# Optimization experiments

Hardware: AMD Instinct MI355X
Metric: run time of the kernel (lower is better)

## Reference

```python
import jax, jax.numpy as jnp
import numpy as np

N_NODES = 10000   # graph size (pos/field tables, dense adjacency)
FEATS = 32        # node_feats
HEADS = 4         # n_heads
SAMPLES = 256     # n_samples (random mids per endpoint)
SENTINELS = 8     # n_sentinels
N_BATCH = 2048    # edges per forward batch
N_EDGES_G = 100000  # graph edges used to build dense adjacency buffer


def setup_inputs() -> dict:
    key = jax.random.key(0)
    ks = jax.random.split(key, 7)
    edge = jax.random.randint(ks[0], (N_BATCH, 2), 0, N_NODES)
    mid0 = jax.random.randint(ks[1], (HEADS, N_BATCH, SAMPLES), 0, N_NODES)
    mid1 = jax.random.randint(ks[2], (HEADS, N_BATCH, SAMPLES), 0, N_NODES)
    # learned parameters (torch: nn.Parameter(torch.rand(...)), ones*5)
    pos = jax.random.uniform(ks[3], (HEADS, N_NODES, FEATS), dtype=jnp.float32)
    field = jax.random.uniform(ks[4], (HEADS, N_NODES, FEATS), dtype=jnp.float32)
    uncertainty = jnp.ones((1, 1, 1), jnp.float32) * 5.0
    # dense adjacency buffer: -1 everywhere, +1 on (symmetrized) graph edges
    src_g = jax.random.randint(ks[5], (N_EDGES_G,), 0, N_NODES)
    dst_g = jax.random.randint(ks[6], (N_EDGES_G,), 0, N_NODES)
    edge_mat = -jnp.ones((N_NODES, N_NODES), jnp.float32)
    edge_mat = edge_mat.at[src_g, dst_g].set(1.0).at[dst_g, src_g].set(1.0)
    return {"edge": edge, "mid0": mid0, "mid1": mid1, "pos": pos,
            "field": field, "uncertainty": uncertainty, "edge_mat": edge_mat}


def reference(edge, mid0, mid1, pos, field, uncertainty, edge_mat):
    src, dst = edge[:, 0], edge[:, 1]
    h = jnp.arange(HEADS)[:, None, None]           # head index for gathers
    # gather sampled mid-node positions and form difference vectors
    srcdiff = pos[:, src][:, :, None, :] - pos[h, mid0]   # (H, n, S, F)
    dstdiff = pos[:, dst][:, :, None, :] - pos[h, mid1]   # (H, n, S, F)
    # per-sample dot-product logits + memory bias (memory == -1 branch)
    logits1 = (jnp.einsum('hnsf,hnf->hns', srcdiff, field[:, dst])
               + uncertainty * edge_mat[mid0, dst[None, :, None]])
    logits2 = (jnp.einsum('hnsf,hnf->hns', dstdiff, field[:, src])
               + uncertainty * edge_mat[src[None, :, None], mid1])
    logits = jnp.concatenate([logits1, logits2], axis=2)  # (H, n, 2S)
    dist = jnp.concatenate([jnp.linalg.norm(srcdiff, axis=3),
                            jnp.linalg.norm(dstdiff, axis=3)], axis=2)
    # sentinels: zero logits at unit distance
    n = edge.shape[0]
    logits = jnp.concatenate([logits, jnp.zeros((HEADS, n, SENTINELS), logits.dtype)], axis=2)
    dist = jnp.concatenate([dist, jnp.ones((HEADS, n, SENTINELS), dist.dtype)], axis=2)
    # softmin aggregation: softmax over (1 - dist), weighted sum of logits, mean over heads
    w = jax.nn.softmax(1.0 - dist, axis=2)                # (H, n, 2S+sent)
    return jnp.sum(logits * w, axis=2).mean(0)            # (n,)
```

## Files before the change

kernel.cpp:

```cpp
#include <hip/hip_runtime.h>

#define N_NODES 10000
#define FEATS 32
#define HEADS 4
#define SAMPLES 256
#define N_BATCH 2048
#define NGROUP 40
#define NWORDS (NGROUP * 4)

typedef float f32x4 __attribute__((ext_vector_type(4)));
typedef unsigned long long u64;

#define WS_NEEDED (N_NODES * NWORDS * 8)

__global__ __launch_bounds__(256) void mask_dedup_kernel(
    const int* __restrict__ edge,
    const float* __restrict__ edge_mat,
    u64* __restrict__ mask_table,
    float* __restrict__ out)
{
    const int bid  = blockIdx.x;
    const int tid  = threadIdx.x;
    const int w    = tid >> 6;
    const int lane = tid & 63;

    if (tid == 0 && bid < N_BATCH) out[bid] = 0.f;

    const int v = edge[bid];

    __shared__ int s_dup;
    if (tid == 0) s_dup = 0;
    __syncthreads();
    for (int j = tid; j < bid; j += 256)
        if (edge[j] == v) s_dup = 1;
    __syncthreads();
    if (s_dup) return;

    const float* rp = edge_mat + (size_t)v * N_NODES;
    u64* wsn = mask_table + (size_t)v * NWORDS;

    f32x4 val[10];
    #pragma unroll
    for (int i = 0; i < 10; ++i) {
        const int base = (i * 4 + w) * 256 + lane * 4;
        f32x4 t = {-1.f, -1.f, -1.f, -1.f};
        if (base < N_NODES) t = *(const f32x4*)(rp + base);
        val[i] = t;
    }
    #pragma unroll
    for (int i = 0; i < 10; ++i) {
        const int g = i * 4 + w;
        u64 b0 = __ballot(val[i].x > 0.f);
        u64 b1 = __ballot(val[i].y > 0.f);
        u64 b2 = __ballot(val[i].z > 0.f);
        u64 b3 = __ballot(val[i].w > 0.f);
        if (lane < 4) {
            u64 bb = lane == 0 ? b0 : lane == 1 ? b1 : lane == 2 ? b2 : b3;
            wsn[g * 4 + lane] = bb;
        }
    }
}

__global__ __launch_bounds__(256, 4) void madgraph_kernel(
    const int* __restrict__ edge,
    const int* __restrict__ mid0,
    const int* __restrict__ mid1,
    const float* __restrict__ pos,
    const float* __restrict__ field,
    const float* __restrict__ unc,
    const u64* __restrict__ mask_table,
    float* __restrict__ out)
{
    const int b    = blockIdx.x;
    const int h    = b & 3;
    const int tid  = threadIdx.x;
    const int w    = tid >> 6;
    const int lane = tid & 63;
    const int n    = (b >> 2) + 512 * w;

    __shared__ u64 s_mask[4][2 * NWORDS];

    const int src = edge[2 * n];
    const int dst = edge[2 * n + 1];
    const float U = unc[0];

    const u64* wdst = mask_table + (size_t)dst * NWORDS;
    const u64* wsrc = mask_table + (size_t)src * NWORDS;
    #pragma unroll
    for (int k = 0; k < 5; ++k) {
        const int idx = k * 64 + lane;
        s_mask[w][idx] = (idx < NWORDS) ? wdst[idx] : wsrc[idx - NWORDS];
    }

    const float* posh   = pos   + (size_t)h * N_NODES * FEATS;
    const float* fieldh = field + (size_t)h * N_NODES * FEATS;
    const int q = lane & 3;
    const int g = lane >> 2;

    float4 A[2][2], F[2][2];
    #pragma unroll
    for (int sd = 0; sd < 2; ++sd) {
        const float4* pa = (const float4*)(posh   + (size_t)(sd ? dst : src) * FEATS);
        const float4* pf = (const float4*)(fieldh + (size_t)(sd ? src : dst) * FEATS);
        A[sd][0] = pa[q]; A[sd][1] = pa[q + 4];
        F[sd][0] = pf[q]; F[sd][1] = pf[q + 4];
    }

    const size_t sb = ((size_t)h * N_BATCH + n) * SAMPLES;
    int mm[8];
    #pragma unroll
    for (int c = 0; c < 8; ++c)
        mm[c] = (c < 4 ? mid0 : mid1)[sb + (c & 3) * 64 + lane];

    float num = 0.f, den = 0.f;
    #pragma unroll
    for (int c = 0; c < 8; ++c) {
        const int side = c >> 2;

        int    mArr[4];
        float4 B0[4], B1[4];
        #pragma unroll
        for (int t = 0; t < 4; ++t)
            mArr[t] = __shfl(mm[c], t * 16 + g);
        #pragma unroll
        for (int t = 0; t < 4; ++t) {
            const float4* rp = (const float4*)(posh + (size_t)mArr[t] * FEATS);
            B0[t] = rp[q];
            B1[t] = rp[q + 4];
        }

        #pragma unroll
        for (int t = 0; t < 4; ++t) {
            float dh = 0.f, nh = 0.f;
            {
                float4 a = A[side][0], f = F[side][0];
                float dx = a.x - B0[t].x, dy = a.y - B0[t].y,
                      dz = a.z - B0[t].z, dw = a.w - B0[t].w;
                dh += dx * f.x + dy * f.y + dz * f.z + dw * f.w;
                nh += dx * dx + dy * dy + dz * dz + dw * dw;
            }
            {
                float4 a = A[side][1], f = F[side][1];
                float dx = a.x - B1[t].x, dy = a.y - B1[t].y,
                      dz = a.z - B1[t].z, dw = a.w - B1[t].w;
                dh += dx * f.x + dy * f.y + dz * f.z + dw * f.w;
                nh += dx * dx + dy * dy + dz * dz + dw * dw;
            }
            dh += __shfl_xor(dh, 1); nh += __shfl_xor(nh, 1);
            dh += __shfl_xor(dh, 2); nh += __shfl_xor(nh, 2);

            const u64 wbits =
                s_mask[w][side * NWORDS + ((mArr[t] >> 8) << 2) + (mArr[t] & 3)];
            const float em = ((wbits >> ((mArr[t] >> 2) & 63)) & 1ull) ? U : -U;

            const float wgt = __expf(1.0f - sqrtf(nh));
            num += (dh + em) * wgt;
            den += wgt;
        }
    }

    #pragma unroll
    for (int off = 32; off > 0; off >>= 1) {
        num += __shfl_xor(num, off);
        den += __shfl_xor(den, off);
    }
    if (lane == 0) {
        atomicAdd(out + n, 0.25f * (num / (den + 32.0f)));
    }
}

__global__ __launch_bounds__(256) void mask_kernel(
    const int* __restrict__ edge,
    const float* __restrict__ edge_mat,
    u64* __restrict__ ws_mask,
    float* __restrict__ out)
{
    const int n    = blockIdx.x;
    const int tid  = threadIdx.x;
    const int wave = tid >> 6;
    const int lane = tid & 63;
    const int src = edge[2 * n];
    const int dst = edge[2 * n + 1];
    if (tid == 0) out[n] = 0.f;
    u64* wsn = ws_mask + (size_t)n * 2 * NWORDS;
    #pragma unroll
    for (int r = 0; r < 2; ++r) {
        const float* rp = edge_mat + (size_t)(r ? src : dst) * N_NODES;
        for (int g = wave; g < NGROUP; g += 4) {
            int base = g * 256 + lane * 4;
            float4 v = make_float4(-1.f, -1.f, -1.f, -1.f);
            if (base < N_NODES) v = *(const float4*)(rp + base);
            u64 b0 = __ballot(v.x > 0.f);
            u64 b1 = __ballot(v.y > 0.f);
            u64 b2 = __ballot(v.z > 0.f);
            u64 b3 = __ballot(v.w > 0.f);
            if (lane < 4) {
                u64 bb = lane == 0 ? b0 : lane == 1 ? b1 : lane == 2 ? b2 : b3;
                wsn[r * NWORDS + g * 4 + lane] = bb;
            }
        }
    }
}

__global__ __launch_bounds__(256, 4) void madgraph_kernel_fb(
    const int* __restrict__ edge,
    const int* __restrict__ mid0,
    const int* __restrict__ mid1,
    const float* __restrict__ pos,
    const float* __restrict__ field,
    const float* __restrict__ unc,
    const u64* __restrict__ ws_mask,
    float* __restrict__ out)
{
    const int b    = blockIdx.x;
    const int h    = b & 3;
    const int tid  = threadIdx.x;
    const int w    = tid >> 6;
    const int lane = tid & 63;
    const int n    = (b >> 2) + 512 * w;

    __shared__ u64 s_mask[4][2 * NWORDS];

    const int src = edge[2 * n];
    const int dst = edge[2 * n + 1];
    const float U = unc[0];

    const u64* wsn = ws_mask + (size_t)n * 2 * NWORDS;
    #pragma unroll
    for (int k = 0; k < 5; ++k)
        s_mask[w][k * 64 + lane] = wsn[k * 64 + lane];

    const float* posh   = pos   + (size_t)h * N_NODES * FEATS;
    const float* fieldh = field + (size_t)h * N_NODES * FEATS;
    const int q = lane & 3;
    const int g = lane >> 2;

    float4 A[2][2], F[2][2];
    #pragma unroll
    for (int sd = 0; sd < 2; ++sd) {
        const float4* pa = (const float4*)(posh   + (size_t)(sd ? dst : src) * FEATS);
        const float4* pf = (const float4*)(fieldh + (size_t)(sd ? src : dst) * FEATS);
        A[sd][0] = pa[q]; A[sd][1] = pa[q + 4];
        F[sd][0] = pf[q]; F[sd][1] = pf[q + 4];
    }

    const size_t sb = ((size_t)h * N_BATCH + n) * SAMPLES;
    int mm[8];
    #pragma unroll
    for (int c = 0; c < 8; ++c)
        mm[c] = (c < 4 ? mid0 : mid1)[sb + (c & 3) * 64 + lane];

    float num = 0.f, den = 0.f;
    #pragma unroll
    for (int c = 0; c < 8; ++c) {
        const int side = c >> 2;
        int    mArr[4];
        float4 B0[4], B1[4];
        #pragma unroll
        for (int t = 0; t < 4; ++t)
            mArr[t] = __shfl(mm[c], t * 16 + g);
        #pragma unroll
        for (int t = 0; t < 4; ++t) {
            const float4* rp = (const float4*)(posh + (size_t)mArr[t] * FEATS);
            B0[t] = rp[q];
            B1[t] = rp[q + 4];
        }
        #pragma unroll
        for (int t = 0; t < 4; ++t) {
            float dh = 0.f, nh = 0.f;
            {
                float4 a = A[side][0], f = F[side][0];
                float dx = a.x - B0[t].x, dy = a.y - B0[t].y,
                      dz = a.z - B0[t].z, dw = a.w - B0[t].w;
                dh += dx * f.x + dy * f.y + dz * f.z + dw * f.w;
                nh += dx * dx + dy * dy + dz * dz + dw * dw;
            }
            {
                float4 a = A[side][1], f = F[side][1];
                float dx = a.x - B1[t].x, dy = a.y - B1[t].y,
                      dz = a.z - B1[t].z, dw = a.w - B1[t].w;
                dh += dx * f.x + dy * f.y + dz * f.z + dw * f.w;
                nh += dx * dx + dy * dy + dz * dz + dw * dw;
            }
            dh += __shfl_xor(dh, 1); nh += __shfl_xor(nh, 1);
            dh += __shfl_xor(dh, 2); nh += __shfl_xor(nh, 2);
            const u64 wbits =
                s_mask[w][side * NWORDS + ((mArr[t] >> 8) << 2) + (mArr[t] & 3)];
            const float em = ((wbits >> ((mArr[t] >> 2) & 63)) & 1ull) ? U : -U;
            const float wgt = __expf(1.0f - sqrtf(nh));
            num += (dh + em) * wgt;
            den += wgt;
        }
    }
    #pragma unroll
    for (int off = 32; off > 0; off >>= 1) {
        num += __shfl_xor(num, off);
        den += __shfl_xor(den, off);
    }
    if (lane == 0)
        atomicAdd(out + n, 0.25f * (num / (den + 32.0f)));
}

extern "C" void kernel_launch(void* const* d_in, const int* in_sizes, int n_in,
                              void* d_out, int out_size, void* d_ws, size_t ws_size,
                              hipStream_t stream) {
    const int*   edge     = (const int*)  d_in[0];
    const int*   mid0     = (const int*)  d_in[1];
    const int*   mid1     = (const int*)  d_in[2];
    const float* pos      = (const float*)d_in[3];
    const float* field    = (const float*)d_in[4];
    const float* unc      = (const float*)d_in[5];
    const float* edge_mat = (const float*)d_in[6];
    float*       out      = (float*)d_out;

    if (ws_size >= (size_t)WS_NEEDED) {
        u64* mask_table = (u64*)d_ws;
        mask_dedup_kernel<<<2 * N_BATCH, 256, 0, stream>>>(edge, edge_mat,
                                                           mask_table, out);
        madgraph_kernel<<<N_BATCH, 256, 0, stream>>>(edge, mid0, mid1, pos,
                                                     field, unc, mask_table, out);
    } else {
        u64* ws_mask = (u64*)d_ws;
        mask_kernel<<<N_BATCH, 256, 0, stream>>>(edge, edge_mat, ws_mask, out);
        madgraph_kernel_fb<<<N_BATCH, 256, 0, stream>>>(edge, mid0, mid1, pos,
                                                        field, unc, ws_mask, out);
    }
}
```

Baseline: 58.64 us.

## Gather mid-node positions from an fp16 copy of pos built in the mask kernel

Adds extra blocks to the mask kernel that convert pos to fp16 in workspace each call. The main kernel then gathers mid-node rows as 16-byte fp16 vectors (8 features per lane, 8 samples per batch), halving the random-gather traffic. It also drops the fallback mask kernel path. The cost is an extra full pos conversion pass every call, and the fp16 rounding of pos adds precision error to distances and logits.

Result: slower. 61.13 us (+4.2%).

```diff
diff --git a/kernel.cpp b/kernel.cpp
--- a/kernel.cpp
+++ b/kernel.cpp
@@ -9,20 +9,43 @@
 #define NWORDS (NGROUP * 4)
 
 typedef float f32x4 __attribute__((ext_vector_type(4)));
+typedef _Float16 f16x8 __attribute__((ext_vector_type(8)));
 typedef unsigned long long u64;
 
-#define WS_NEEDED (N_NODES * NWORDS * 8)
+#define WS_P16_OFF  12800000
+#define WS_NEED_V2  15360000
+#define WS_NEED_V1  12800000
+#define POS_ELEMS   (HEADS * N_NODES * FEATS)
 
 __global__ __launch_bounds__(256) void mask_dedup_kernel(
     const int* __restrict__ edge,
     const float* __restrict__ edge_mat,
+    const float* __restrict__ pos,
     u64* __restrict__ mask_table,
-    float* __restrict__ out)
+    _Float16* __restrict__ ws_pos16,
+    float* __restrict__ out,
+    int do_conv)
 {
     const int bid  = blockIdx.x;
     const int tid  = threadIdx.x;
     const int w    = tid >> 6;
     const int lane = tid & 63;
+
+    if (bid >= 2 * N_BATCH) {
+        if (!do_conv) return;
+        const int idx = (bid - 2 * N_BATCH) * 2048 + tid * 8;
+        if (idx < POS_ELEMS) {
+            const float4 v0 = *(const float4*)(pos + idx);
+            const float4 v1 = *(const float4*)(pos + idx + 4);
+            f16x8 o;
+            o[0] = (_Float16)v0.x; o[1] = (_Float16)v0.y;
+            o[2] = (_Float16)v0.z; o[3] = (_Float16)v0.w;
+            o[4] = (_Float16)v1.x; o[5] = (_Float16)v1.y;
+            o[6] = (_Float16)v1.z; o[7] = (_Float16)v1.w;
+            *(f16x8*)(ws_pos16 + idx) = o;
+        }
+        return;
+    }
 
     if (tid == 0 && bid < N_BATCH) out[bid] = 0.f;
 
@@ -61,7 +84,118 @@
     }
 }
 
-__global__ __launch_bounds__(256, 4) void madgraph_kernel(
+__global__ __launch_bounds__(256, 4) void madgraph_v2(
+    const int* __restrict__ edge,
+    const int* __restrict__ mid0,
+    const int* __restrict__ mid1,
+    const float* __restrict__ pos,
+    const float* __restrict__ field,
+    const float* __restrict__ unc,
+    const u64* __restrict__ mask_table,
+    const _Float16* __restrict__ ws_pos16,
+    float* __restrict__ out)
+{
+    const int b    = blockIdx.x;
+    const int h    = b & 3;
+    const int tid  = threadIdx.x;
+    const int w    = tid >> 6;
+    const int lane = tid & 63;
+    const int n    = (b >> 2) + 512 * w;
+
+    __shared__ u64 s_mask[4][2 * NWORDS];
+
+    const int src = edge[2 * n];
+    const int dst = edge[2 * n + 1];
+    const float U = unc[0];
+
+    const u64* wdst = mask_table + (size_t)dst * NWORDS;
+    const u64* wsrc = mask_table + (size_t)src * NWORDS;
+    #pragma unroll
+    for (int k = 0; k < 5; ++k) {
+        const int idx = k * 64 + lane;
+        s_mask[w][idx] = (idx < NWORDS) ? wdst[idx] : wsrc[idx - NWORDS];
+    }
+
+    const float*    posh   = pos      + (size_t)h * N_NODES * FEATS;
+    const float*    fieldh = field    + (size_t)h * N_NODES * FEATS;
+    const _Float16* p16h   = ws_pos16 + (size_t)h * N_NODES * FEATS;
+
+    const int q = lane & 3;
+    const int g = lane >> 2;
+
+    float4 A[2][2], F[2][2];
+    #pragma unroll
+    for (int sd = 0; sd < 2; ++sd) {
+        const float4* pa = (const float4*)(posh   + (size_t)(sd ? dst : src) * FEATS) + q * 2;
+        const float4* pf = (const float4*)(fieldh + (size_t)(sd ? src : dst) * FEATS) + q * 2;
+        A[sd][0] = pa[0]; A[sd][1] = pa[1];
+        F[sd][0] = pf[0]; F[sd][1] = pf[1];
+    }
+
+    const size_t sb = ((size_t)h * N_BATCH + n) * SAMPLES;
+    int mm[8];
+    #pragma unroll
+    for (int c = 0; c < 8; ++c)
+        mm[c] = (c < 4 ? mid0 : mid1)[sb + (c & 3) * 64 + lane];
+
+    float num = 0.f, den = 0.f;
+
+    #pragma unroll
+    for (int cc = 0; cc < 4; ++cc) {
+        const int side = cc >> 1;
+
+        int   mA[8];
+        f16x8 B[8];
+        #pragma unroll
+        for (int t = 0; t < 4; ++t) {
+            mA[t]     = __shfl(mm[2 * cc],     t * 16 + g);
+            mA[4 + t] = __shfl(mm[2 * cc + 1], t * 16 + g);
+        }
+        #pragma unroll
+        for (int t = 0; t < 8; ++t)
+            B[t] = *(const f16x8*)(p16h + (size_t)mA[t] * FEATS + q * 8);
+
+        #pragma unroll
+        for (int t = 0; t < 8; ++t) {
+            float dh = 0.f, nh = 0.f;
+            {
+                float4 a = A[side][0], f = F[side][0];
+                float dx = a.x - (float)B[t][0], dy = a.y - (float)B[t][1],
+                      dz = a.z - (float)B[t][2], dw = a.w - (float)B[t][3];
+                dh += dx * f.x + dy * f.y + dz * f.z + dw * f.w;
+                nh += dx * dx + dy * dy + dz * dz + dw * dw;
+            }
+            {
+                float4 a = A[side][1], f = F[side][1];
+                float dx = a.x - (float)B[t][4], dy = a.y - (float)B[t][5],
+                      dz = a.z - (float)B[t][6], dw = a.w - (float)B[t][7];
+                dh += dx * f.x + dy * f.y + dz * f.z + dw * f.w;
+                nh += dx * dx + dy * dy + dz * dz + dw * dw;
+            }
+            dh += __shfl_xor(dh, 1); nh += __shfl_xor(nh, 1);
+            dh += __shfl_xor(dh, 2); nh += __shfl_xor(nh, 2);
+
+            const u64 wbits =
+                s_mask[w][side * NWORDS + ((mA[t] >> 8) << 2) + (mA[t] & 3)];
+            const float em = ((wbits >> ((mA[t] >> 2) & 63)) & 1ull) ? U : -U;
+
+            const float wgt = __expf(1.0f - sqrtf(nh));
+            num += (dh + em) * wgt;
+            den += wgt;
+        }
+    }
+
+    #pragma unroll
+    for (int off = 32; off > 0; off >>= 1) {
+        num += __shfl_xor(num, off);
+        den += __shfl_xor(den, off);
+    }
+    if (lane == 0) {
+        atomicAdd(out + n, 0.25f * (num / (den + 32.0f)));
+    }
+}
+
+__global__ __launch_bounds__(256, 4) void madgraph_v1(
     const int* __restrict__ edge,
     const int* __restrict__ mid0,
     const int* __restrict__ mid1,
@@ -91,144 +225,6 @@
         const int idx = k * 64 + lane;
         s_mask[w][idx] = (idx < NWORDS) ? wdst[idx] : wsrc[idx - NWORDS];
     }
-
-    const float* posh   = pos   + (size_t)h * N_NODES * FEATS;
-    const float* fieldh = field + (size_t)h * N_NODES * FEATS;
-    const int q = lane & 3;
-    const int g = lane >> 2;
-
-    float4 A[2][2], F[2][2];
-    #pragma unroll
-    for (int sd = 0; sd < 2; ++sd) {
-        const float4* pa = (const float4*)(posh   + (size_t)(sd ? dst : src) * FEATS);
-        const float4* pf = (const float4*)(fieldh + (size_t)(sd ? src : dst) * FEATS);
-        A[sd][0] = pa[q]; A[sd][1] = pa[q + 4];
-        F[sd][0] = pf[q]; F[sd][1] = pf[q + 4];
-    }
-
-    const size_t sb = ((size_t)h * N_BATCH + n) * SAMPLES;
-    int mm[8];
-    #pragma unroll
-    for (int c = 0; c < 8; ++c)
-        mm[c] = (c < 4 ? mid0 : mid1)[sb + (c & 3) * 64 + lane];
-
-    float num = 0.f, den = 0.f;
-    #pragma unroll
-    for (int c = 0; c < 8; ++c) {
-        const int side = c >> 2;
-
-        int    mArr[4];
-        float4 B0[4], B1[4];
-        #pragma unroll
-        for (int t = 0; t < 4; ++t)
-            mArr[t] = __shfl(mm[c], t * 16 + g);
-        #pragma unroll
-        for (int t = 0; t < 4; ++t) {
-            const float4* rp = (const float4*)(posh + (size_t)mArr[t] * FEATS);
-            B0[t] = rp[q];
-            B1[t] = rp[q + 4];
-        }
-
-        #pragma unroll
-        for (int t = 0; t < 4; ++t) {
-            float dh = 0.f, nh = 0.f;
-            {
-                float4 a = A[side][0], f = F[side][0];
-                float dx = a.x - B0[t].x, dy = a.y - B0[t].y,
-                      dz = a.z - B0[t].z, dw = a.w - B0[t].w;
-                dh += dx * f.x + dy * f.y + dz * f.z + dw * f.w;
-                nh += dx * dx + dy * dy + dz * dz + dw * dw;
-            }
-            {
-                float4 a = A[side][1], f = F[side][1];
-                float dx = a.x - B1[t].x, dy = a.y - B1[t].y,
-                      dz = a.z - B1[t].z, dw = a.w - B1[t].w;
-                dh += dx * f.x + dy * f.y + dz * f.z + dw * f.w;
-                nh += dx * dx + dy * dy + dz * dz + dw * dw;
-            }
-            dh += __shfl_xor(dh, 1); nh += __shfl_xor(nh, 1);
-            dh += __shfl_xor(dh, 2); nh += __shfl_xor(nh, 2);
-
-            const u64 wbits =
-                s_mask[w][side * NWORDS + ((mArr[t] >> 8) << 2) + (mArr[t] & 3)];
-            const float em = ((wbits >> ((mArr[t] >> 2) & 63)) & 1ull) ? U : -U;
-
-            const float wgt = __expf(1.0f - sqrtf(nh));
-            num += (dh + em) * wgt;
-            den += wgt;
-        }
-    }
-
-    #pragma unroll
-    for (int off = 32; off > 0; off >>= 1) {
-        num += __shfl_xor(num, off);
-        den += __shfl_xor(den, off);
-    }
-    if (lane == 0) {
-        atomicAdd(out + n, 0.25f * (num / (den + 32.0f)));
-    }
-}
-
-__global__ __launch_bounds__(256) void mask_kernel(
-    const int* __restrict__ edge,
-    const float* __restrict__ edge_mat,
-    u64* __restrict__ ws_mask,
-    float* __restrict__ out)
-{
-    const int n    = blockIdx.x;
-    const int tid  = threadIdx.x;
-    const int wave = tid >> 6;
-    const int lane = tid & 63;
-    const int src = edge[2 * n];
-    const int dst = edge[2 * n + 1];
-    if (tid == 0) out[n] = 0.f;
-    u64* wsn = ws_mask + (size_t)n * 2 * NWORDS;
-    #pragma unroll
-    for (int r = 0; r < 2; ++r) {
-        const float* rp = edge_mat + (size_t)(r ? src : dst) * N_NODES;
-        for (int g = wave; g < NGROUP; g += 4) {
-            int base = g * 256 + lane * 4;
-            float4 v = make_float4(-1.f, -1.f, -1.f, -1.f);
-            if (base < N_NODES) v = *(const float4*)(rp + base);
-            u64 b0 = __ballot(v.x > 0.f);
-            u64 b1 = __ballot(v.y > 0.f);
-            u64 b2 = __ballot(v.z > 0.f);
-            u64 b3 = __ballot(v.w > 0.f);
-            if (lane < 4) {
-                u64 bb = lane == 0 ? b0 : lane == 1 ? b1 : lane == 2 ? b2 : b3;
-                wsn[r * NWORDS + g * 4 + lane] = bb;
-            }
-        }
-    }
-}
-
-__global__ __launch_bounds__(256, 4) void madgraph_kernel_fb(
-    const int* __restrict__ edge,
-    const int* __restrict__ mid0,
-    const int* __restrict__ mid1,
-    const float* __restrict__ pos,
-    const float* __restrict__ field,
-    const float* __restrict__ unc,
-    const u64* __restrict__ ws_mask,
-    float* __restrict__ out)
-{
-    const int b    = blockIdx.x;
-    const int h    = b & 3;
-    const int tid  = threadIdx.x;
-    const int w    = tid >> 6;
-    const int lane = tid & 63;
-    const int n    = (b >> 2) + 512 * w;
-
-    __shared__ u64 s_mask[4][2 * NWORDS];
-
-    const int src = edge[2 * n];
-    const int dst = edge[2 * n + 1];
-    const float U = unc[0];
-
-    const u64* wsn = ws_mask + (size_t)n * 2 * NWORDS;
-    #pragma unroll
-    for (int k = 0; k < 5; ++k)
-        s_mask[w][k * 64 + lane] = wsn[k * 64 + lane];
 
     const float* posh   = pos   + (size_t)h * N_NODES * FEATS;
     const float* fieldh = field + (size_t)h * N_NODES * FEATS;
@@ -313,16 +309,18 @@
     const float* edge_mat = (const float*)d_in[6];
     float*       out      = (float*)d_out;
 
-    if (ws_size >= (size_t)WS_NEEDED) {
-        u64* mask_table = (u64*)d_ws;
-        mask_dedup_kernel<<<2 * N_BATCH, 256, 0, stream>>>(edge, edge_mat,
-                                                           mask_table, out);
-        madgraph_kernel<<<N_BATCH, 256, 0, stream>>>(edge, mid0, mid1, pos,
-                                                     field, unc, mask_table, out);
+    u64*      mask_table = (u64*)d_ws;
+    _Float16* ws_pos16   = (_Float16*)((char*)d_ws + WS_P16_OFF);
+    const int v2 = ws_size >= (size_t)WS_NEED_V2;
+
+    mask_dedup_kernel<<<2 * N_BATCH + 640, 256, 0, stream>>>(
+        edge, edge_mat, pos, mask_table, ws_pos16, out, v2);
+
+    if (v2) {
+        madgraph_v2<<<N_BATCH, 256, 0, stream>>>(edge, mid0, mid1, pos, field,
+                                                 unc, mask_table, ws_pos16, out);
     } else {
-        u64* ws_mask = (u64*)d_ws;
-        mask_kernel<<<N_BATCH, 256, 0, stream>>>(edge, edge_mat, ws_mask, out);
-        madgraph_kernel_fb<<<N_BATCH, 256, 0, stream>>>(edge, mid0, mid1, pos,
-                                                        field, unc, ws_mask, out);
+        madgraph_v1<<<N_BATCH, 256, 0, stream>>>(edge, mid0, mid1, pos, field,
+                                                 unc, mask_table, out);
     }
 }
```
